# Optimization experiments

Measured on AMD Instinct MI355X. Metric: run time of the kernel, lower is better.

Reference implementation:

```python
import jax, jax.numpy as jnp
import numpy as np

N = 50000      # num_nodes
E = 800000     # num_edges
D = 128        # hidden_dim
POOL_RATIO = 0.5
CROSS_W = 1.0  # cross_weight


def _gcn(x, W, b, src, dst, n):
    """GCNConv: symmetric-normalized aggregation with self-loops. Dropout is identity (eval)."""
    loops = jnp.arange(n)
    s = jnp.concatenate([src, loops])
    d = jnp.concatenate([dst, loops])
    deg = jax.ops.segment_sum(jnp.ones(s.shape, x.dtype), d, num_segments=n)
    inv_sqrt = jax.lax.rsqrt(jnp.maximum(deg, 1.0))  # deg >= 1 due to self-loops
    xw = x @ W                                        # [n, D]
    msg = xw[s] * (inv_sqrt[s] * inv_sqrt[d])[:, None]  # [E+n, D] gather
    return jax.ops.segment_sum(msg, d, num_segments=n) + b


def _prelu(x, a):
    return jnp.where(x >= 0, x, a * x)


def setup_inputs() -> dict:
    key = jax.random.key(0)
    ks = jax.random.split(key, 8)
    glorot = lambda k, sh: jax.random.normal(k, sh, jnp.float32) * np.float32(np.sqrt(2.0 / (sh[0] + sh[1])))
    return {
        "feat": jax.random.normal(ks[0], (N, D), jnp.float32),
        "h_neg": jax.random.normal(ks[1], (N, D), jnp.float32),
        "edge_index": jax.random.randint(ks[2], (2, E), 0, N),
        "Wd": glorot(ks[3], (D, D)),
        "bd": jnp.zeros((D,), jnp.float32),
        "prelu_a": jnp.full((1,), 0.25, jnp.float32),
        "Wbil": glorot(ks[4], (D, D)),
        "bbil": jnp.zeros((1,), jnp.float32),
        "Wg1": glorot(ks[5], (D, D)),
        "bg1": jnp.zeros((D,), jnp.float32),
        "Wg2": glorot(ks[6], (D, D)),
        "bg2": jnp.zeros((D,), jnp.float32),
        "Wg3": glorot(ks[7], (D, D)),
        "bg3": jnp.zeros((D,), jnp.float32),
    }


def reference(feat, h_neg, edge_index, Wd, bd, prelu_a, Wbil, bbil,
              Wg1, bg1, Wg2, bg2, Wg3, bg3):
    src, dst = edge_index[0], edge_index[1]
    # --- IndexSelect: dense layer on pos/neg features ---
    h_pos = _prelu(feat @ Wd + bd, prelu_a)
    h_neg_d = _prelu(h_neg @ Wd + bd, prelu_a)
    embed = _gcn(h_pos, Wg1, bg1, src, dst, N)
    h_center = jax.nn.sigmoid(embed)
    # Discriminator (bilinear) positive scores -> node importance
    score_pos = jnp.einsum('nd,de,ne->n', h_pos, Wbil, h_center) + bbil[0]
    _ = jnp.einsum('nd,de,ne->n', h_neg_d, Wbil, h_center) + bbil[0]  # score_neg (logits branch)
    scores = jax.nn.sigmoid(score_pos)
    order = jnp.argsort(-scores)           # descending
    k = int(POOL_RATIO * N)
    select_idx = order[:k]
    select_scores = scores[order][:k]
    # --- GraphPool (use_gcn=True): down-sample GCN, gather, scale ---
    pooled = _gcn(embed, Wg2, bg2, src, dst, N)[select_idx] * select_scores[:, None]
    # --- GraphUnpool: scatter into zeros, up-sample GCN ---
    fine = jnp.zeros((N, D), feat.dtype).at[select_idx].set(pooled)
    out = _gcn(fine, Wg3, bg3, src, dst, N)
    # --- cross/fuse connection ---
    return out + CROSS_W * embed
```

## Files before the change

### kernel.cpp

```cpp
#include <hip/hip_runtime.h>
#include <hip/hip_bf16.h>

#define NN 50000
#define NE 800000
#define DD 128
#define KSEL 25000
#define NBK 391
#define NBLKA 98

typedef unsigned int uint32;
typedef unsigned short ushort16;

__device__ __forceinline__ float sigmoidf(float x){ return 1.f/(1.f+__expf(-x)); }

__device__ __forceinline__ unsigned short f2b(float f){
  union{float f; unsigned u;} v; v.f=f;
  unsigned r=(v.u + 0x7fffu + ((v.u>>16)&1u))>>16;
  return (unsigned short)r;
}

__device__ __forceinline__ void addbf2(float&lo,float&hi,uint32 u,float w){
  lo+=__uint_as_float(u<<16)*w;
  hi+=__uint_as_float(u&0xffff0000u)*w;
}

__global__ __launch_bounds__(1024) void k_bcount(const int* __restrict__ dst,
    int* __restrict__ btot, int* __restrict__ blkcnt){
  __shared__ int h[NBK];
  int tid=threadIdx.x;
  for(int i=tid;i<NBK;i+=1024) h[i]=0;
  __syncthreads();
  int e0=blockIdx.x*8192;
  #pragma unroll
  for(int t=0;t<8;t++){
    int e=e0+t*1024+tid;
    if(e<NE) atomicAdd(&h[dst[e]>>7],1);
  }
  __syncthreads();
  for(int i=tid;i<NBK;i+=1024){
    int c=h[i];
    blkcnt[blockIdx.x*NBK+i]=c;
    if(c) atomicAdd(&btot[i],c);
  }
}

__global__ __launch_bounds__(512) void k_bscan(const int* __restrict__ btot,
    int* __restrict__ boff, const int* __restrict__ blkcnt, int* __restrict__ blkbase,
    int* __restrict__ row_start){
  __shared__ int sdata[512];
  int tid=threadIdx.x;
  int v=(tid<NBK)?btot[tid]:0;
  sdata[tid]=v; __syncthreads();
  for(int off=1;off<512;off<<=1){
    int y=(tid>=off)?sdata[tid-off]:0;
    __syncthreads();
    sdata[tid]+=y;
    __syncthreads();
  }
  int excl=sdata[tid]-v;
  if(tid<NBK) boff[tid]=excl;
  if(tid==NBK-1){ boff[NBK]=excl+v; row_start[NN]=NE; }
  if(tid<NBK){
    int run=excl;
    for(int b=0;b<NBLKA;b++){
      int c=blkcnt[b*NBK+tid];
      blkbase[b*NBK+tid]=run;
      run+=c;
    }
  }
}

__global__ __launch_bounds__(1024) void k_bscatter(const int* __restrict__ src,
    const int* __restrict__ dst, const int* __restrict__ blkbase, uint2* __restrict__ pairs){
  __shared__ int cur[NBK];
  int tid=threadIdx.x;
  for(int i=tid;i<NBK;i+=1024) cur[i]=blkbase[blockIdx.x*NBK+i];
  __syncthreads();
  int e0=blockIdx.x*8192;
  #pragma unroll
  for(int t=0;t<8;t++){
    int e=e0+t*1024+tid;
    if(e<NE){
      int d=dst[e];
      int p=atomicAdd(&cur[d>>7],1);
      uint2 pr; pr.x=(unsigned)src[e]; pr.y=(unsigned)d;
      pairs[p]=pr;
    }
  }
}

__global__ __launch_bounds__(256) void k_bfinal(const uint2* __restrict__ pairs,
    const int* __restrict__ boff, int* __restrict__ row_start,
    float* __restrict__ inv_sq, int* __restrict__ csr_src){
  __shared__ int degl[128];
  __shared__ int cur[128];
  __shared__ int ssum[2];
  int b=blockIdx.x, tid=threadIdx.x;
  int lo=boff[b], hi=boff[b+1];
  if(tid<128) degl[tid]=0;
  __syncthreads();
  for(int e=lo+tid;e<hi;e+=256) atomicAdd(&degl[pairs[e].y&127],1);
  __syncthreads();
  int v=0,x=0;
  if(tid<128){
    v=degl[tid]; x=v;
    #pragma unroll
    for(int off=1;off<64;off<<=1){
      int y=__shfl_up(x,off,64);
      if((tid&63)>=off) x+=y;
    }
    if((tid&63)==63) ssum[tid>>6]=x;
  }
  __syncthreads();
  if(tid<128){
    int incl=x+((tid>=64)?ssum[0]:0);
    int node=b*128+tid;
    int excl=lo+incl-v;
    if(node<NN){
      row_start[node]=excl;
      cur[tid]=excl;
      inv_sq[node]=1.f/sqrtf((float)(v+1));
    }
  }
  __syncthreads();
  for(int e=lo+tid;e<hi;e+=256){
    uint2 pr=pairs[e];
    int p=atomicAdd(&cur[pr.y&127],1);
    csr_src[p]=(int)pr.x;
  }
}

__global__ void k_transpose(const float* __restrict__ W, float* __restrict__ Wt){
  int idx=blockIdx.x*256+threadIdx.x;
  if(idx<DD*DD){
    int k=idx>>7, c=idx&127;
    Wt[idx]=W[c*DD+k];
  }
}

template<int IN_SIG,int ACT,int OUT_BF16,int FUSE_SCORE>
__global__ __launch_bounds__(256) void k_gemm128(const float* __restrict__ A,
    const float* __restrict__ W, const float* __restrict__ bias,
    float* __restrict__ outf, ushort16* __restrict__ outb,
    const float* __restrict__ aparam, const float* __restrict__ hp,
    const float* __restrict__ bbil, float* __restrict__ score){
  __shared__ float Al[128][132];
  int tid=threadIdx.x;
  int row0=blockIdx.x*128;
  {
    const float4* A4=(const float4*)(A+(size_t)row0*DD);
    #pragma unroll
    for(int i=0;i<16;i++){
      int idx=i*256+tid;
      int r=idx>>5, c=(idx&31)*4;
      float4 v=make_float4(0.f,0.f,0.f,0.f);
      if(row0+r<NN) v=A4[idx];
      if(IN_SIG){ v.x=sigmoidf(v.x); v.y=sigmoidf(v.y); v.z=sigmoidf(v.z); v.w=sigmoidf(v.w); }
      *(float4*)&Al[r][c]=v;
    }
  }
  __syncthreads();
  int tx=tid&15, ty=tid>>4;
  float acc[8][8];
  #pragma unroll
  for(int i=0;i<8;i++)
    #pragma unroll
    for(int c=0;c<8;c++) acc[i][c]=0.f;

  for(int k=0;k<DD;k+=4){
    float wv[4][8];
    #pragma unroll
    for(int r=0;r<4;r++){
      float4 lo=*(const float4*)&W[(size_t)(k+r)*DD+tx*8];
      float4 hi=*(const float4*)&W[(size_t)(k+r)*DD+tx*8+4];
      wv[r][0]=lo.x; wv[r][1]=lo.y; wv[r][2]=lo.z; wv[r][3]=lo.w;
      wv[r][4]=hi.x; wv[r][5]=hi.y; wv[r][6]=hi.z; wv[r][7]=hi.w;
    }
    #pragma unroll
    for(int i=0;i<8;i++){
      float4 a=*(const float4*)&Al[ty+16*i][k];
      #pragma unroll
      for(int c=0;c<8;c++)
        acc[i][c]+=a.x*wv[0][c]+a.y*wv[1][c]+a.z*wv[2][c]+a.w*wv[3][c];
    }
  }

  if(FUSE_SCORE){
    float bb=bbil[0];
    #pragma unroll
    for(int i=0;i<8;i++){
      int r=row0+ty+16*i;
      float p=0.f;
      if(r<NN){
        float4 h0=*(const float4*)&hp[(size_t)r*DD+tx*8];
        float4 h1=*(const float4*)&hp[(size_t)r*DD+tx*8+4];
        p=acc[i][0]*h0.x+acc[i][1]*h0.y+acc[i][2]*h0.z+acc[i][3]*h0.w
         +acc[i][4]*h1.x+acc[i][5]*h1.y+acc[i][6]*h1.z+acc[i][7]*h1.w;
      }
      p+=__shfl_xor(p,1,64); p+=__shfl_xor(p,2,64);
      p+=__shfl_xor(p,4,64); p+=__shfl_xor(p,8,64);
      if(tx==0 && r<NN) score[r]=sigmoidf(p+bb);
    }
    return;
  }
  float bl[8]={0,0,0,0,0,0,0,0};
  if(bias){
    float4 b0=*(const float4*)&bias[tx*8];
    float4 b1=*(const float4*)&bias[tx*8+4];
    bl[0]=b0.x; bl[1]=b0.y; bl[2]=b0.z; bl[3]=b0.w;
    bl[4]=b1.x; bl[5]=b1.y; bl[6]=b1.z; bl[7]=b1.w;
  }
  float ap=ACT?aparam[0]:0.f;
  #pragma unroll
  for(int i=0;i<8;i++){
    int r=row0+ty+16*i;
    if(r<NN){
      float o[8];
      #pragma unroll
      for(int c=0;c<8;c++){
        float t=acc[i][c]+bl[c];
        if(ACT) t=t>=0.f?t:ap*t;
        o[c]=t;
      }
      if(OUT_BF16){
        uint4 pk;
        pk.x=((uint32)f2b(o[1])<<16)|f2b(o[0]);
        pk.y=((uint32)f2b(o[3])<<16)|f2b(o[2]);
        pk.z=((uint32)f2b(o[5])<<16)|f2b(o[4]);
        pk.w=((uint32)f2b(o[7])<<16)|f2b(o[6]);
        *(uint4*)&outb[(size_t)r*DD+tx*8]=pk;
      } else {
        float4 q0; q0.x=o[0]; q0.y=o[1]; q0.z=o[2]; q0.w=o[3];
        float4 q1; q1.x=o[4]; q1.y=o[5]; q1.z=o[6]; q1.w=o[7];
        *(float4*)&outf[(size_t)r*DD+tx*8]=q0;
        *(float4*)&outf[(size_t)r*DD+tx*8+4]=q1;
      }
    }
  }
}

__global__ __launch_bounds__(256) void k_agg_f32(const float* __restrict__ xw,
    const int* __restrict__ row_start, const int* __restrict__ csr,
    const float* __restrict__ inv, const float* __restrict__ bias,
    float* __restrict__ outp){
  int node=blockIdx.x*4+(threadIdx.x>>6);
  if(node>=NN) return;
  int lane=threadIdx.x&63;
  int g=lane>>5, li=lane&31;
  int rs=row_start[node], re=row_start[node+1];
  float a0=0.f,a1=0.f,a2=0.f,a3=0.f;
  int j=rs;
  for(; j+3<re; j+=4){
    int sA=csr[j+g], sB=csr[j+2+g];
    float wA=inv[sA], wB=inv[sB];
    float4 vA=*(const float4*)&xw[(size_t)sA*DD+li*4];
    float4 vB=*(const float4*)&xw[(size_t)sB*DD+li*4];
    a0+=vA.x*wA+vB.x*wB; a1+=vA.y*wA+vB.y*wB;
    a2+=vA.z*wA+vB.z*wB; a3+=vA.w*wA+vB.w*wB;
  }
  for(; j+1<re; j+=2){
    int s=csr[j+g];
    float w=inv[s];
    float4 v=*(const float4*)&xw[(size_t)s*DD+li*4];
    a0+=v.x*w; a1+=v.y*w; a2+=v.z*w; a3+=v.w*w;
  }
  if(j<re && g==0){
    int s=csr[j]; float w=inv[s];
    float4 v=*(const float4*)&xw[(size_t)s*DD+li*4];
    a0+=v.x*w; a1+=v.y*w; a2+=v.z*w; a3+=v.w*w;
  }
  if(g==0){
    float wd=inv[node];
    float4 v=*(const float4*)&xw[(size_t)node*DD+li*4];
    a0+=v.x*wd; a1+=v.y*wd; a2+=v.z*wd; a3+=v.w*wd;
  }
  a0+=__shfl_xor(a0,32,64); a1+=__shfl_xor(a1,32,64);
  a2+=__shfl_xor(a2,32,64); a3+=__shfl_xor(a3,32,64);
  if(g==0){
    float wn=inv[node];
    float4 bv=*(const float4*)&bias[li*4];
    float4 o;
    o.x=a0*wn+bv.x; o.y=a1*wn+bv.y; o.z=a2*wn+bv.z; o.w=a3*wn+bv.w;
    *(float4*)&outp[(size_t)node*DD+li*4]=o;
  }
}

template<int MODE>
__global__ __launch_bounds__(256) void k_agg_b16(const uint32* __restrict__ xwb,
    const int* __restrict__ row_start, const int* __restrict__ csr,
    const float* __restrict__ inv, const float* __restrict__ bias,
    float* __restrict__ outp, const float* __restrict__ score,
    const unsigned char* __restrict__ sel, const float* __restrict__ addbuf){
  int node=blockIdx.x*4+(threadIdx.x>>6);
  if(node>=NN) return;
  int lane=threadIdx.x&63;
  if(MODE==1 && !sel[node]){
    float2 z; z.x=0.f; z.y=0.f;
    *(float2*)&outp[(size_t)node*DD+lane*2]=z;
    return;
  }
  int g=lane>>4, li=lane&15;
  int rs=row_start[node], re=row_start[node+1];
  float a[8];
  #pragma unroll
  for(int c=0;c<8;c++) a[c]=0.f;
  int j=rs;
  for(; j+7<re; j+=8){
    int sA=csr[j+g], sB=csr[j+4+g];
    if(MODE!=2 || sel[sA]){
      float w=inv[sA];
      uint4 u=*(const uint4*)(xwb+(size_t)sA*64+li*4);
      addbf2(a[0],a[1],u.x,w); addbf2(a[2],a[3],u.y,w);
      addbf2(a[4],a[5],u.z,w); addbf2(a[6],a[7],u.w,w);
    }
    if(MODE!=2 || sel[sB]){
      float w=inv[sB];
      uint4 u=*(const uint4*)(xwb+(size_t)sB*64+li*4);
      addbf2(a[0],a[1],u.x,w); addbf2(a[2],a[3],u.y,w);
      addbf2(a[4],a[5],u.z,w); addbf2(a[6],a[7],u.w,w);
    }
  }
  for(; j+3<re; j+=4){
    int s=csr[j+g];
    if(MODE!=2 || sel[s]){
      float w=inv[s];
      uint4 u=*(const uint4*)(xwb+(size_t)s*64+li*4);
      addbf2(a[0],a[1],u.x,w); addbf2(a[2],a[3],u.y,w);
      addbf2(a[4],a[5],u.z,w); addbf2(a[6],a[7],u.w,w);
    }
  }
  int rem=re-j;
  if(g<rem){
    int s=csr[j+g];
    if(MODE!=2 || sel[s]){
      float w=inv[s];
      uint4 u=*(const uint4*)(xwb+(size_t)s*64+li*4);
      addbf2(a[0],a[1],u.x,w); addbf2(a[2],a[3],u.y,w);
      addbf2(a[4],a[5],u.z,w); addbf2(a[6],a[7],u.w,w);
    }
  }
  if(g==0 && (MODE!=2 || sel[node])){
    float wd=inv[node];
    uint4 u=*(const uint4*)(xwb+(size_t)node*64+li*4);
    addbf2(a[0],a[1],u.x,wd); addbf2(a[2],a[3],u.y,wd);
    addbf2(a[4],a[5],u.z,wd); addbf2(a[6],a[7],u.w,wd);
  }
  #pragma unroll
  for(int c=0;c<8;c++){
    a[c]+=__shfl_xor(a[c],16,64);
    a[c]+=__shfl_xor(a[c],32,64);
  }
  if(g<2){
    float wn=inv[node];
    int cb=li*8+g*4;
    float4 bv=*(const float4*)&bias[cb];
    float r0=a[g*4+0]*wn+bv.x, r1=a[g*4+1]*wn+bv.y;
    float r2=a[g*4+2]*wn+bv.z, r3=a[g*4+3]*wn+bv.w;
    if(MODE==1){
      float sc=score[node];
      r0*=sc; r1*=sc; r2*=sc; r3*=sc;
    } else {
      float4 ad=*(const float4*)&addbuf[(size_t)node*DD+cb];
      r0+=ad.x; r1+=ad.y; r2+=ad.z; r3+=ad.w;
    }
    float4 o; o.x=r0; o.y=r1; o.z=r2; o.w=r3;
    *(float4*)&outp[(size_t)node*DD+cb]=o;
  }
}

template<int NB,int PASS>
__global__ __launch_bounds__(256) void k_hist(const float* __restrict__ score,
    int* __restrict__ ghist, const int* __restrict__ ctrl){
  __shared__ int lh[NB];
  int tid=threadIdx.x;
  for(int i=tid;i<NB;i+=256) lh[i]=0;
  __syncthreads();
  int p0=0,p01=0;
  if(PASS==1) p0=ctrl[0];
  if(PASS==2) p01=ctrl[2];
  for(int i=blockIdx.x*256+tid; i<NN; i+=gridDim.x*256){
    unsigned b=__float_as_uint(score[i]);
    if(PASS==0) atomicAdd(&lh[b>>20],1);
    else if(PASS==1){ if((int)(b>>20)==p0) atomicAdd(&lh[(b>>8)&0xFFF],1); }
    else { if((int)(b>>8)==p01) atomicAdd(&lh[b&0xFF],1); }
  }
  __syncthreads();
  for(int i=tid;i<NB;i+=256){ int v=lh[i]; if(v) atomicAdd(&ghist[i],v); }
}

template<int NB,int PASS>
__global__ void k_findb(const int* __restrict__ hist, int* __restrict__ ctrl){
  const int NT=NB/4;
  __shared__ int gsum[NT];
  int t=threadIdx.x;
  int s=hist[t*4]+hist[t*4+1]+hist[t*4+2]+hist[t*4+3];
  int x=s; gsum[t]=x; __syncthreads();
  for(int off=1;off<NT;off<<=1){
    int y=(t+off<NT)?gsum[t+off]:0;
    __syncthreads();
    x+=y; gsum[t]=x; __syncthreads();
  }
  int base;
  if(PASS==0) base=0; else if(PASS==1) base=ctrl[1]; else base=ctrl[3];
  int above=base+((t<NT-1)?gsum[t+1]:0);
  int incl=base+gsum[t];
  if(above<KSEL && incl>=KSEL){
    int c=above, B=0;
    for(int b=3;b>=0;b--){
      int hb=hist[t*4+b];
      if(c+hb>=KSEL){ B=t*4+b; break; }
      c+=hb;
    }
    if(PASS==0){ ctrl[0]=B; ctrl[1]=c; }
    else if(PASS==1){ ctrl[2]=(ctrl[0]<<12)|B; ctrl[3]=c; }
    else { ctrl[4]=(int)((((unsigned)ctrl[2])<<8)|(unsigned)B); ctrl[5]=KSEL-c; }
  }
}

__global__ void k_sel(const float* __restrict__ score, int* __restrict__ ctrl,
                      int* __restrict__ tie_list, unsigned char* __restrict__ sel){
  int i=blockIdx.x*256+threadIdx.x;
  if(i>=NN) return;
  unsigned b=__float_as_uint(score[i]);
  unsigned thr=(unsigned)ctrl[4];
  if(b>thr){ sel[i]=1; }
  else if(b==thr){
    sel[i]=0;
    int p=atomicAdd(&ctrl[6],1);
    if(p<4096) tie_list[p]=i;
  } else sel[i]=0;
}

__global__ __launch_bounds__(256) void k_tie(const int* __restrict__ ctrl,
    const int* __restrict__ tie_list, unsigned char* __restrict__ sel){
  int m=ctrl[6]; if(m>4096) m=4096;
  int needed=ctrl[5];
  for(int t=threadIdx.x; t<m; t+=blockDim.x){
    int idx=tie_list[t];
    int rank=0;
    for(int j=0;j<m;j++) rank+=(tie_list[j]<idx)?1:0;
    if(rank<needed) sel[idx]=1;
  }
}

extern "C" void kernel_launch(void* const* d_in, const int* in_sizes, int n_in,
                              void* d_out, int out_size, void* d_ws, size_t ws_size,
                              hipStream_t stream){
  const float* feat   =(const float*)d_in[0];
  const int*   ei     =(const int*)  d_in[2];
  const int*   src    = ei;
  const int*   dst    = ei + NE;
  const float* Wd     =(const float*)d_in[3];
  const float* bd     =(const float*)d_in[4];
  const float* prelu_a=(const float*)d_in[5];
  const float* Wbil   =(const float*)d_in[6];
  const float* bbil   =(const float*)d_in[7];
  const float* Wg1    =(const float*)d_in[8];
  const float* bg1    =(const float*)d_in[9];
  const float* Wg2    =(const float*)d_in[10];
  const float* bg2    =(const float*)d_in[11];
  const float* Wg3    =(const float*)d_in[12];
  const float* bg3    =(const float*)d_in[13];
  float* out=(float*)d_out;

  char* p=(char*)d_ws;
  auto alloc=[&](size_t bytes)->void*{ void* r=(void*)p; p+=((bytes+255)/256)*256; return r; };
  float* h_pos   =(float*)alloc((size_t)NN*DD*4);
  float* embed   =(float*)alloc((size_t)NN*DD*4);
  float* xw      =(float*)alloc((size_t)NN*DD*4);
  float* score   =(float*)alloc((size_t)NN*4);
  float* inv_sq  =(float*)alloc((size_t)NN*4);
  float* WbT     =(float*)alloc((size_t)DD*DD*4);
  int*   row_st  =(int*)  alloc((size_t)(NN+1)*4);
  int*   csr_src =(int*)  alloc((size_t)NE*4);
  int*   ctrl    =(int*)  alloc(64);
  int*   hist0   =(int*)  alloc(4096*4);
  int*   hist1   =(int*)  alloc(4096*4);
  int*   hist2   =(int*)  alloc(256*4);
  int*   tie_list=(int*)  alloc(4096*4);
  unsigned char* sel=(unsigned char*)alloc(NN);
  int*   btot    =(int*)  alloc((size_t)NBK*4);
  int*   boff    =(int*)  alloc((size_t)(NBK+1)*4);
  int*   blkcnt  =(int*)  alloc((size_t)NBLKA*NBK*4);
  int*   blkbase =(int*)  alloc((size_t)NBLKA*NBK*4);
  uint2* pairs   =(uint2*)xw;
  ushort16* xwb  =(ushort16*)xw;
  float* fine = out;

  const int NB=(NN+255)/256;
  const int GB=(NN+127)/128;
  const int AB=(NN+3)/4;

  hipMemsetAsync(ctrl, 0, (size_t)((char*)tie_list-(char*)ctrl), stream);
  hipMemsetAsync(btot, 0, (size_t)NBK*4, stream);

  k_bcount  <<<NBLKA,1024,0,stream>>>(dst, btot, blkcnt);
  k_bscan   <<<1,512,0,stream>>>(btot, boff, blkcnt, blkbase, row_st);
  k_bscatter<<<NBLKA,1024,0,stream>>>(src, dst, blkbase, pairs);
  k_bfinal  <<<NBK,256,0,stream>>>(pairs, boff, row_st, inv_sq, csr_src);
  k_transpose<<<64,256,0,stream>>>(Wbil, WbT);

  k_gemm128<0,1,0,0><<<GB,256,0,stream>>>(feat, Wd, bd, h_pos, nullptr, prelu_a, nullptr, nullptr, nullptr);
  k_gemm128<0,0,0,0><<<GB,256,0,stream>>>(h_pos, Wg1, nullptr, xw, nullptr, nullptr, nullptr, nullptr, nullptr);
  k_agg_f32<<<AB,256,0,stream>>>(xw, row_st, csr_src, inv_sq, bg1, embed);
  k_gemm128<1,0,0,1><<<GB,256,0,stream>>>(embed, WbT, nullptr, nullptr, nullptr, nullptr, h_pos, bbil, score);
  k_hist<4096,0><<<64,256,0,stream>>>(score, hist0, ctrl);
  k_findb<4096,0><<<1,1024,0,stream>>>(hist0, ctrl);
  k_hist<4096,1><<<64,256,0,stream>>>(score, hist1, ctrl);
  k_findb<4096,1><<<1,1024,0,stream>>>(hist1, ctrl);
  k_hist<256,2><<<64,256,0,stream>>>(score, hist2, ctrl);
  k_findb<256,2><<<1,64,0,stream>>>(hist2, ctrl);
  k_sel<<<NB,256,0,stream>>>(score, ctrl, tie_list, sel);
  k_tie<<<1,256,0,stream>>>(ctrl, tie_list, sel);
  k_gemm128<0,0,1,0><<<GB,256,0,stream>>>(embed, Wg2, nullptr, nullptr, xwb, nullptr, nullptr, nullptr, nullptr);
  k_agg_b16<1><<<AB,256,0,stream>>>((const uint32*)xwb, row_st, csr_src, inv_sq, bg2, fine, score, sel, nullptr);
  k_gemm128<0,0,1,0><<<GB,256,0,stream>>>(fine, Wg3, nullptr, nullptr, xwb, nullptr, nullptr, nullptr, nullptr);
  k_agg_b16<2><<<AB,256,0,stream>>>((const uint32*)xwb, row_st, csr_src, inv_sq, bg3, out, nullptr, sel, embed);
}
```

Baseline: 373.2 us.

## Partition CSR edges by source chunk and aggregate in source-chunk-ordered passes

```diff
diff --git a/kernel.cpp b/kernel.cpp
--- a/kernel.cpp
+++ b/kernel.cpp
@@ -7,6 +7,10 @@
 #define KSEL 25000
 #define NBK 391
 #define NBLKA 98
+#define NCH 13
+#define PBLK 768
+#define PTH 512
+#define NPB 66
 
 typedef unsigned int uint32;
 typedef unsigned short ushort16;
@@ -17,11 +21,6 @@
   union{float f; unsigned u;} v; v.f=f;
   unsigned r=(v.u + 0x7fffu + ((v.u>>16)&1u))>>16;
   return (unsigned short)r;
-}
-
-__device__ __forceinline__ void addbf2(float&lo,float&hi,uint32 u,float w){
-  lo+=__uint_as_float(u<<16)*w;
-  hi+=__uint_as_float(u&0xffff0000u)*w;
 }
 
 __global__ __launch_bounds__(1024) void k_bcount(const int* __restrict__ dst,
@@ -45,8 +44,7 @@
 }
 
 __global__ __launch_bounds__(512) void k_bscan(const int* __restrict__ btot,
-    int* __restrict__ boff, const int* __restrict__ blkcnt, int* __restrict__ blkbase,
-    int* __restrict__ row_start){
+    int* __restrict__ boff, const int* __restrict__ blkcnt, int* __restrict__ blkbase){
   __shared__ int sdata[512];
   int tid=threadIdx.x;
   int v=(tid<NBK)?btot[tid]:0;
@@ -59,7 +57,7 @@
   }
   int excl=sdata[tid]-v;
   if(tid<NBK) boff[tid]=excl;
-  if(tid==NBK-1){ boff[NBK]=excl+v; row_start[NN]=NE; }
+  if(tid==NBK-1) boff[NBK]=excl+v;
   if(tid<NBK){
     int run=excl;
     for(int b=0;b<NBLKA;b++){
@@ -90,20 +88,25 @@
 }
 
 __global__ __launch_bounds__(256) void k_bfinal(const uint2* __restrict__ pairs,
-    const int* __restrict__ boff, int* __restrict__ row_start,
+    const int* __restrict__ boff, int* __restrict__ rowptr,
     float* __restrict__ inv_sq, int* __restrict__ csr_src){
-  __shared__ int degl[128];
-  __shared__ int cur[128];
+  __shared__ int cnt[128*NCH];
+  __shared__ int cur[128*NCH];
   __shared__ int ssum[2];
   int b=blockIdx.x, tid=threadIdx.x;
   int lo=boff[b], hi=boff[b+1];
-  if(tid<128) degl[tid]=0;
-  __syncthreads();
-  for(int e=lo+tid;e<hi;e+=256) atomicAdd(&degl[pairs[e].y&127],1);
+  for(int i=tid;i<128*NCH;i+=256) cnt[i]=0;
+  __syncthreads();
+  for(int e=lo+tid;e<hi;e+=256){
+    uint2 pr=pairs[e];
+    atomicAdd(&cnt[(pr.y&127)*NCH+(pr.x>>12)],1);
+  }
   __syncthreads();
   int v=0,x=0;
   if(tid<128){
-    v=degl[tid]; x=v;
+    #pragma unroll
+    for(int c=0;c<NCH;c++) v+=cnt[tid*NCH+c];
+    x=v;
     #pragma unroll
     for(int off=1;off<64;off<<=1){
       int y=__shfl_up(x,off,64);
@@ -115,17 +118,22 @@
   if(tid<128){
     int incl=x+((tid>=64)?ssum[0]:0);
     int node=b*128+tid;
-    int excl=lo+incl-v;
     if(node<NN){
-      row_start[node]=excl;
-      cur[tid]=excl;
+      int run=lo+incl-v;
       inv_sq[node]=1.f/sqrtf((float)(v+1));
+      #pragma unroll
+      for(int c=0;c<NCH;c++){
+        rowptr[node*(NCH+1)+c]=run;
+        cur[tid*NCH+c]=run;
+        run+=cnt[tid*NCH+c];
+      }
+      rowptr[node*(NCH+1)+NCH]=run;
     }
   }
   __syncthreads();
   for(int e=lo+tid;e<hi;e+=256){
     uint2 pr=pairs[e];
-    int p=atomicAdd(&cur[pr.y&127],1);
+    int p=atomicAdd(&cur[(pr.y&127)*NCH+(pr.x>>12)],1);
     csr_src[p]=(int)pr.x;
   }
 }
@@ -239,132 +247,95 @@
   }
 }
 
-__global__ __launch_bounds__(256) void k_agg_f32(const float* __restrict__ xw,
-    const int* __restrict__ row_start, const int* __restrict__ csr,
-    const float* __restrict__ inv, const float* __restrict__ bias,
-    float* __restrict__ outp){
-  int node=blockIdx.x*4+(threadIdx.x>>6);
-  if(node>=NN) return;
-  int lane=threadIdx.x&63;
-  int g=lane>>5, li=lane&31;
-  int rs=row_start[node], re=row_start[node+1];
-  float a0=0.f,a1=0.f,a2=0.f,a3=0.f;
-  int j=rs;
-  for(; j+3<re; j+=4){
-    int sA=csr[j+g], sB=csr[j+2+g];
-    float wA=inv[sA], wB=inv[sB];
-    float4 vA=*(const float4*)&xw[(size_t)sA*DD+li*4];
-    float4 vB=*(const float4*)&xw[(size_t)sB*DD+li*4];
-    a0+=vA.x*wA+vB.x*wB; a1+=vA.y*wA+vB.y*wB;
-    a2+=vA.z*wA+vB.z*wB; a3+=vA.w*wA+vB.w*wB;
-  }
-  for(; j+1<re; j+=2){
-    int s=csr[j+g];
-    float w=inv[s];
-    float4 v=*(const float4*)&xw[(size_t)s*DD+li*4];
-    a0+=v.x*w; a1+=v.y*w; a2+=v.z*w; a3+=v.w*w;
-  }
-  if(j<re && g==0){
-    int s=csr[j]; float w=inv[s];
-    float4 v=*(const float4*)&xw[(size_t)s*DD+li*4];
-    a0+=v.x*w; a1+=v.y*w; a2+=v.z*w; a3+=v.w*w;
-  }
-  if(g==0){
-    float wd=inv[node];
-    float4 v=*(const float4*)&xw[(size_t)node*DD+li*4];
-    a0+=v.x*wd; a1+=v.y*wd; a2+=v.z*wd; a3+=v.w*wd;
-  }
-  a0+=__shfl_xor(a0,32,64); a1+=__shfl_xor(a1,32,64);
-  a2+=__shfl_xor(a2,32,64); a3+=__shfl_xor(a3,32,64);
-  if(g==0){
-    float wn=inv[node];
-    float4 bv=*(const float4*)&bias[li*4];
-    float4 o;
-    o.x=a0*wn+bv.x; o.y=a1*wn+bv.y; o.z=a2*wn+bv.z; o.w=a3*wn+bv.w;
-    *(float4*)&outp[(size_t)node*DD+li*4]=o;
-  }
-}
-
 template<int MODE>
-__global__ __launch_bounds__(256) void k_agg_b16(const uint32* __restrict__ xwb,
-    const int* __restrict__ row_start, const int* __restrict__ csr,
+__global__ __launch_bounds__(PTH) void k_aggp(const void* __restrict__ xwv,
+    const int* __restrict__ rowptr, const int* __restrict__ csr,
     const float* __restrict__ inv, const float* __restrict__ bias,
     float* __restrict__ outp, const float* __restrict__ score,
     const unsigned char* __restrict__ sel, const float* __restrict__ addbuf){
-  int node=blockIdx.x*4+(threadIdx.x>>6);
-  if(node>=NN) return;
-  int lane=threadIdx.x&63;
-  if(MODE==1 && !sel[node]){
-    float2 z; z.x=0.f; z.y=0.f;
-    *(float2*)&outp[(size_t)node*DD+lane*2]=z;
-    return;
-  }
-  int g=lane>>4, li=lane&15;
-  int rs=row_start[node], re=row_start[node+1];
-  float a[8];
-  #pragma unroll
-  for(int c=0;c<8;c++) a[c]=0.f;
-  int j=rs;
-  for(; j+7<re; j+=8){
-    int sA=csr[j+g], sB=csr[j+4+g];
-    if(MODE!=2 || sel[sA]){
-      float w=inv[sA];
-      uint4 u=*(const uint4*)(xwb+(size_t)sA*64+li*4);
-      addbf2(a[0],a[1],u.x,w); addbf2(a[2],a[3],u.y,w);
-      addbf2(a[4],a[5],u.z,w); addbf2(a[6],a[7],u.w,w);
-    }
-    if(MODE!=2 || sel[sB]){
-      float w=inv[sB];
-      uint4 u=*(const uint4*)(xwb+(size_t)sB*64+li*4);
-      addbf2(a[0],a[1],u.x,w); addbf2(a[2],a[3],u.y,w);
-      addbf2(a[4],a[5],u.z,w); addbf2(a[6],a[7],u.w,w);
-    }
-  }
-  for(; j+3<re; j+=4){
-    int s=csr[j+g];
-    if(MODE!=2 || sel[s]){
-      float w=inv[s];
-      uint4 u=*(const uint4*)(xwb+(size_t)s*64+li*4);
-      addbf2(a[0],a[1],u.x,w); addbf2(a[2],a[3],u.y,w);
-      addbf2(a[4],a[5],u.z,w); addbf2(a[6],a[7],u.w,w);
-    }
-  }
-  int rem=re-j;
-  if(g<rem){
-    int s=csr[j+g];
-    if(MODE!=2 || sel[s]){
-      float w=inv[s];
-      uint4 u=*(const uint4*)(xwb+(size_t)s*64+li*4);
-      addbf2(a[0],a[1],u.x,w); addbf2(a[2],a[3],u.y,w);
-      addbf2(a[4],a[5],u.z,w); addbf2(a[6],a[7],u.w,w);
-    }
-  }
-  if(g==0 && (MODE!=2 || sel[node])){
-    float wd=inv[node];
-    uint4 u=*(const uint4*)(xwb+(size_t)node*64+li*4);
-    addbf2(a[0],a[1],u.x,wd); addbf2(a[2],a[3],u.y,wd);
-    addbf2(a[4],a[5],u.z,wd); addbf2(a[6],a[7],u.w,wd);
-  }
-  #pragma unroll
-  for(int c=0;c<8;c++){
-    a[c]+=__shfl_xor(a[c],16,64);
-    a[c]+=__shfl_xor(a[c],32,64);
-  }
-  if(g<2){
-    float wn=inv[node];
-    int cb=li*8+g*4;
-    float4 bv=*(const float4*)&bias[cb];
-    float r0=a[g*4+0]*wn+bv.x, r1=a[g*4+1]*wn+bv.y;
-    float r2=a[g*4+2]*wn+bv.z, r3=a[g*4+3]*wn+bv.w;
+  __shared__ float acc[NPB][DD];
+  int tid=threadIdx.x, w=tid>>6, lane=tid&63;
+  int g=lane>>5, li=lane&31;
+  int base=blockIdx.x*NPB;
+  for(int i=tid;i<NPB*DD/4;i+=PTH) ((float4*)&acc[0][0])[i]=make_float4(0.f,0.f,0.f,0.f);
+  __syncthreads();
+  const float* xwf=(const float*)xwv;
+  const uint32* xwb=(const uint32*)xwv;
+  for(int c=0;c<NCH;c++){
+    for(int nl=w;nl<NPB;nl+=8){
+      int n=base+nl; if(n>=NN) break;
+      if(MODE==1 && !sel[n]) continue;
+      int p0=rowptr[n*(NCH+1)+c], p1=rowptr[n*(NCH+1)+c+1];
+      bool self=((n>>12)==c) && (MODE!=2 || sel[n]);
+      if(p0>=p1 && !self) continue;
+      float a0=0.f,a1=0.f;
+      int j=p0;
+      if(MODE==0){
+        for(; j+1<p1; j+=2){
+          int s0=csr[j], s1=csr[j+1];
+          float w0=inv[s0], w1=inv[s1];
+          float2 v0=*(const float2*)&xwf[(size_t)s0*DD+g*64+li*2];
+          float2 v1=*(const float2*)&xwf[(size_t)s1*DD+g*64+li*2];
+          a0+=v0.x*w0+v1.x*w1; a1+=v0.y*w0+v1.y*w1;
+        }
+        if(j<p1){
+          int s=csr[j]; float wt=inv[s];
+          float2 v=*(const float2*)&xwf[(size_t)s*DD+g*64+li*2];
+          a0+=v.x*wt; a1+=v.y*wt;
+        }
+        if(self){
+          float wt=inv[n];
+          float2 v=*(const float2*)&xwf[(size_t)n*DD+g*64+li*2];
+          a0+=v.x*wt; a1+=v.y*wt;
+        }
+      } else {
+        for(; j+1<p1; j+=2){
+          int s0=csr[j], s1=csr[j+1];
+          bool t0=(MODE!=2)||sel[s0], t1=(MODE!=2)||sel[s1];
+          uint32 u0=t0?xwb[(size_t)s0*64+g*32+li]:0u;
+          uint32 u1=t1?xwb[(size_t)s1*64+g*32+li]:0u;
+          float w0=t0?inv[s0]:0.f, w1=t1?inv[s1]:0.f;
+          a0+=__uint_as_float(u0<<16)*w0+__uint_as_float(u1<<16)*w1;
+          a1+=__uint_as_float(u0&0xffff0000u)*w0+__uint_as_float(u1&0xffff0000u)*w1;
+        }
+        if(j<p1){
+          int s=csr[j];
+          if(MODE!=2 || sel[s]){
+            float wt=inv[s];
+            uint32 u=xwb[(size_t)s*64+g*32+li];
+            a0+=__uint_as_float(u<<16)*wt; a1+=__uint_as_float(u&0xffff0000u)*wt;
+          }
+        }
+        if(self){
+          float wt=inv[n];
+          uint32 u=xwb[(size_t)n*64+g*32+li];
+          a0+=__uint_as_float(u<<16)*wt; a1+=__uint_as_float(u&0xffff0000u)*wt;
+        }
+      }
+      int col=g*64+li*2;
+      float2 t=*(float2*)&acc[nl][col];
+      t.x+=a0; t.y+=a1;
+      *(float2*)&acc[nl][col]=t;
+    }
+  }
+  for(int nl=w;nl<NPB;nl+=8){
+    int n=base+nl; if(n>=NN) break;
+    int col=lane*2;
+    float2 t=*(const float2*)&acc[nl][col];
+    float wn=inv[n];
+    float2 bv=*(const float2*)&bias[col];
+    float r0,r1;
     if(MODE==1){
-      float sc=score[node];
-      r0*=sc; r1*=sc; r2*=sc; r3*=sc;
+      if(!sel[n]){ r0=0.f; r1=0.f; }
+      else { float sc=score[n]; r0=(t.x*wn+bv.x)*sc; r1=(t.y*wn+bv.y)*sc; }
+    } else if(MODE==2){
+      float2 ad=*(const float2*)&addbuf[(size_t)n*DD+col];
+      r0=t.x*wn+bv.x+ad.x; r1=t.y*wn+bv.y+ad.y;
     } else {
-      float4 ad=*(const float4*)&addbuf[(size_t)node*DD+cb];
-      r0+=ad.x; r1+=ad.y; r2+=ad.z; r3+=ad.w;
-    }
-    float4 o; o.x=r0; o.y=r1; o.z=r2; o.w=r3;
-    *(float4*)&outp[(size_t)node*DD+cb]=o;
+      r0=t.x*wn+bv.x; r1=t.y*wn+bv.y;
+    }
+    float2 o; o.x=r0; o.y=r1;
+    *(float2*)&outp[(size_t)n*DD+col]=o;
   }
 }
 
@@ -471,7 +442,7 @@
   float* score   =(float*)alloc((size_t)NN*4);
   float* inv_sq  =(float*)alloc((size_t)NN*4);
   float* WbT     =(float*)alloc((size_t)DD*DD*4);
-  int*   row_st  =(int*)  alloc((size_t)(NN+1)*4);
+  int*   rowptr  =(int*)  alloc((size_t)NN*(NCH+1)*4);
   int*   csr_src =(int*)  alloc((size_t)NE*4);
   int*   ctrl    =(int*)  alloc(64);
   int*   hist0   =(int*)  alloc(4096*4);
@@ -489,20 +460,19 @@
 
   const int NB=(NN+255)/256;
   const int GB=(NN+127)/128;
-  const int AB=(NN+3)/4;
 
   hipMemsetAsync(ctrl, 0, (size_t)((char*)tie_list-(char*)ctrl), stream);
   hipMemsetAsync(btot, 0, (size_t)NBK*4, stream);
 
   k_bcount  <<<NBLKA,1024,0,stream>>>(dst, btot, blkcnt);
-  k_bscan   <<<1,512,0,stream>>>(btot, boff, blkcnt, blkbase, row_st);
+  k_bscan   <<<1,512,0,stream>>>(btot, boff, blkcnt, blkbase);
   k_bscatter<<<NBLKA,1024,0,stream>>>(src, dst, blkbase, pairs);
-  k_bfinal  <<<NBK,256,0,stream>>>(pairs, boff, row_st, inv_sq, csr_src);
+  k_bfinal  <<<NBK,256,0,stream>>>(pairs, boff, rowptr, inv_sq, csr_src);
   k_transpose<<<64,256,0,stream>>>(Wbil, WbT);
 
   k_gemm128<0,1,0,0><<<GB,256,0,stream>>>(feat, Wd, bd, h_pos, nullptr, prelu_a, nullptr, nullptr, nullptr);
   k_gemm128<0,0,0,0><<<GB,256,0,stream>>>(h_pos, Wg1, nullptr, xw, nullptr, nullptr, nullptr, nullptr, nullptr);
-  k_agg_f32<<<AB,256,0,stream>>>(xw, row_st, csr_src, inv_sq, bg1, embed);
+  k_aggp<0><<<PBLK,PTH,0,stream>>>(xw, rowptr, csr_src, inv_sq, bg1, embed, nullptr, nullptr, nullptr);
   k_gemm128<1,0,0,1><<<GB,256,0,stream>>>(embed, WbT, nullptr, nullptr, nullptr, nullptr, h_pos, bbil, score);
   k_hist<4096,0><<<64,256,0,stream>>>(score, hist0, ctrl);
   k_findb<4096,0><<<1,1024,0,stream>>>(hist0, ctrl);
@@ -513,7 +483,7 @@
   k_sel<<<NB,256,0,stream>>>(score, ctrl, tie_list, sel);
   k_tie<<<1,256,0,stream>>>(ctrl, tie_list, sel);
   k_gemm128<0,0,1,0><<<GB,256,0,stream>>>(embed, Wg2, nullptr, nullptr, xwb, nullptr, nullptr, nullptr, nullptr);
-  k_agg_b16<1><<<AB,256,0,stream>>>((const uint32*)xwb, row_st, csr_src, inv_sq, bg2, fine, score, sel, nullptr);
+  k_aggp<1><<<PBLK,PTH,0,stream>>>(xwb, rowptr, csr_src, inv_sq, bg2, fine, score, sel, nullptr);
   k_gemm128<0,0,1,0><<<GB,256,0,stream>>>(fine, Wg3, nullptr, nullptr, xwb, nullptr, nullptr, nullptr, nullptr);
-  k_agg_b16<2><<<AB,256,0,stream>>>((const uint32*)xwb, row_st, csr_src, inv_sq, bg3, out, nullptr, sel, embed);
-}
+  k_aggp<2><<<PBLK,PTH,0,stream>>>(xwb, rowptr, csr_src, inv_sq, bg3, out, nullptr, sel, embed);
+}
```

Result: slower. 634.4 us (+70.0%).
